# Kernel optimization log

Measured on AMD Instinct MI355X. Metric: run time of the kernel, lower is better.

The kernel has to match this reference:

```python
import jax, jax.numpy as jnp
import numpy as np

B, S, D, H = 2, 2048, 1024, 16
ND = D // H  # head dim = 64


def setup_inputs() -> dict:
    key = jax.random.key(0)
    ks = jax.random.split(key, 11)
    scale = 1.0 / np.sqrt(D)
    inp = {
        "q": jax.random.normal(ks[0], (B, S, D), dtype=jnp.float32),
        "k": jax.random.normal(ks[1], (B, S, D), dtype=jnp.float32),
        "v": jax.random.normal(ks[2], (B, S, D), dtype=jnp.float32),
        # causal mask, broadcast over batch and heads
        "mask": jnp.tril(jnp.ones((S, S), dtype=jnp.int32))[None, None, :, :],
        "Wq": jax.random.normal(ks[3], (D, D), dtype=jnp.float32) * scale,
        "bq": jnp.zeros((D,), dtype=jnp.float32),
        "Wk": jax.random.normal(ks[4], (D, D), dtype=jnp.float32) * scale,
        "bk": jnp.zeros((D,), dtype=jnp.float32),
        "Wv": jax.random.normal(ks[5], (D, D), dtype=jnp.float32) * scale,
        "bv": jnp.zeros((D,), dtype=jnp.float32),
        "Wo": jax.random.normal(ks[6], (D, D), dtype=jnp.float32) * scale,
        "bo": jnp.zeros((D,), dtype=jnp.float32),
    }
    return inp


def reference(q, k, v, mask, Wq, bq, Wk, bk, Wv, bv, Wo, bo):
    batch, seq_len, _ = q.shape
    # torch nn.Linear: x @ W.T + b
    qh = (q @ Wq.T + bq).reshape(batch, seq_len, H, ND).transpose(0, 2, 1, 3)
    kh = (k @ Wk.T + bk).reshape(batch, seq_len, H, ND).transpose(0, 2, 1, 3)
    vh = (v @ Wv.T + bv).reshape(batch, seq_len, H, ND).transpose(0, 2, 1, 3)
    # [B,H,S,S] scores
    score = jnp.einsum("bhqd,bhkd->bhqk", qh, kh) / jnp.sqrt(jnp.float32(ND))
    score = jnp.where(mask == 0, jnp.float32(-1e9), score)
    score = jax.nn.softmax(score, axis=-1)
    out = jnp.einsum("bhqk,bhkd->bhqd", score, vh)
    out = out.transpose(0, 2, 1, 3).reshape(batch, seq_len, D)
    return out @ Wo.T + bo
```

## Files before the change

kernel.cpp:

```cpp
#include <hip/hip_runtime.h>
#include <hip/hip_bf16.h>
#include <stdint.h>

#define S_LEN 2048
#define DMODEL 1024
#define NHEAD 16
#define HDIM 64
#define BATCH 2

typedef __bf16 bf16_t;
typedef __attribute__((ext_vector_type(8))) __bf16 bf16x8;
typedef __attribute__((ext_vector_type(4))) __bf16 bf16x4;
typedef __attribute__((ext_vector_type(4))) float f32x4;

#define LOG2E 1.44269504088896340736f

__device__ __forceinline__ void gload_lds16(const void* g, void* l) {
  __builtin_amdgcn_global_load_lds(
      (const __attribute__((address_space(1))) uint32_t*)g,
      (__attribute__((address_space(3))) uint32_t*)l, 16, 0, 0);
}

__global__ __launch_bounds__(256) void convert_all(
    const float* __restrict__ q, const float* __restrict__ k, const float* __restrict__ v,
    const float* __restrict__ wq, const float* __restrict__ wk, const float* __restrict__ wv,
    const float* __restrict__ wo,
    bf16_t* __restrict__ qb, bf16_t* __restrict__ kb, bf16_t* __restrict__ vb,
    bf16_t* __restrict__ wqb, bf16_t* __restrict__ wkb, bf16_t* __restrict__ wvb,
    bf16_t* __restrict__ wob)
{
  const size_t M1 = 1048576;
  size_t e = ((size_t)blockIdx.x * 256 + threadIdx.x) * 4;
  const float* src; bf16_t* dst; size_t off;
  if      (e <  4*M1) { src = q;  dst = qb;  off = e;         }
  else if (e <  8*M1) { src = k;  dst = kb;  off = e - 4*M1;  }
  else if (e < 12*M1) { src = v;  dst = vb;  off = e - 8*M1;  }
  else if (e < 13*M1) { src = wq; dst = wqb; off = e - 12*M1; }
  else if (e < 14*M1) { src = wk; dst = wkb; off = e - 13*M1; }
  else if (e < 15*M1) { src = wv; dst = wvb; off = e - 14*M1; }
  else                { src = wo; dst = wob; off = e - 15*M1; }
  float4 f = *reinterpret_cast<const float4*>(src + off);
  bf16x4 o;
  o[0] = (bf16_t)f.x; o[1] = (bf16_t)f.y; o[2] = (bf16_t)f.z; o[3] = (bf16_t)f.w;
  *reinterpret_cast<bf16x4*>(dst + off) = o;
}

__device__ __forceinline__ void gemm_body(
    const bf16_t* __restrict__ A, const bf16_t* __restrict__ W,
    const float* __restrict__ bias, bf16_t* __restrict__ outb,
    float* __restrict__ outf, int M, int N, int K, float scale, int packmode)
{
  __shared__ bf16_t As[128 * 32];
  __shared__ bf16_t Bs[128 * 32];
  int tid = threadIdx.x;
  int w = tid >> 6, lane = tid & 63;
  int lr = lane & 15, lg = lane >> 4;
  int wr = w >> 1, wc = w & 1;
  int m0 = blockIdx.x * 128, n0 = blockIdx.y * 128;

  f32x4 acc[4][4];
#pragma unroll
  for (int a = 0; a < 4; ++a)
#pragma unroll
    for (int bq = 0; bq < 4; ++bq) acc[a][bq] = (f32x4){0.f, 0.f, 0.f, 0.f};

  int col_st = (lane & 3) * 8;

  for (int kt = 0; kt < K; kt += 32) {
#pragma unroll
    for (int it = 0; it < 2; ++it) {
      int chunkbase = (w * 2 + it) * 512;
      int row = (w * 2 + it) * 16 + (lane >> 2);
      gload_lds16(A + (size_t)(m0 + row) * K + kt + col_st, &As[chunkbase]);
      gload_lds16(W + (size_t)(n0 + row) * K + kt + col_st, &Bs[chunkbase]);
    }
    __syncthreads();
    bf16x8 af[4], bfv[4];
#pragma unroll
    for (int mf = 0; mf < 4; ++mf)
      af[mf] = *reinterpret_cast<const bf16x8*>(&As[(wr * 64 + mf * 16 + lr) * 32 + lg * 8]);
#pragma unroll
    for (int nf = 0; nf < 4; ++nf)
      bfv[nf] = *reinterpret_cast<const bf16x8*>(&Bs[(wc * 64 + nf * 16 + lr) * 32 + lg * 8]);
#pragma unroll
    for (int mf = 0; mf < 4; ++mf)
#pragma unroll
      for (int nf = 0; nf < 4; ++nf)
        acc[mf][nf] = __builtin_amdgcn_mfma_f32_16x16x32_bf16(af[mf], bfv[nf], acc[mf][nf], 0, 0, 0);
    __syncthreads();
  }

#pragma unroll
  for (int mf = 0; mf < 4; ++mf) {
#pragma unroll
    for (int nf = 0; nf < 4; ++nf) {
      int col = n0 + wc * 64 + nf * 16 + lr;
      float bcol = bias[col];
#pragma unroll
      for (int i = 0; i < 4; ++i) {
        int row = m0 + wr * 64 + mf * 16 + lg * 4 + i;
        float vv = (acc[mf][nf][i] + bcol) * scale;
        if (outf) {
          outf[(size_t)row * N + col] = vv;
        } else if (packmode == 0) {
          outb[(size_t)row * N + col] = (bf16_t)vv;
        } else if (packmode == 1) {
          int hh = col >> 6, dh = col & 63;
          int half = dh >> 5, klg = (dh >> 3) & 3, j = dh & 7;
          int bb = row >> 11, s = row & 2047;
          size_t off = ((((size_t)(bb * 16 + hh) * 32 + (s >> 6)) * 4 + ((s >> 4) & 3)) * 2 + half) * 512
                     + (klg * 16 + (s & 15)) * 8 + j;
          outb[off] = (bf16_t)vv;
        } else {
          int hh = col >> 6, d = col & 63;
          int dfo = d >> 4, vlr = d & 15;
          int bb = row >> 11, s = row & 2047;
          int t64 = s >> 6, sin_ = s & 63;
          int half = sin_ >> 5, vlg = (sin_ >> 3) & 3, j = s & 7;
          size_t off = (((size_t)(bb * 16 + hh) * 32 + t64) * 8 + dfo * 2 + half) * 512
                     + (vlg * 16 + vlr) * 8 + j;
          outb[off] = (bf16_t)vv;
        }
      }
    }
  }
}

__global__ __launch_bounds__(256) void gemm_proj(
    const bf16_t* __restrict__ qb, const bf16_t* __restrict__ kb, const bf16_t* __restrict__ vb,
    const bf16_t* __restrict__ wqb, const bf16_t* __restrict__ wkb, const bf16_t* __restrict__ wvb,
    const float* __restrict__ bq, const float* __restrict__ bk, const float* __restrict__ bv,
    bf16_t* __restrict__ Qp, bf16_t* __restrict__ Kpk, bf16_t* __restrict__ Vpk)
{
  int z = blockIdx.z;
  const bf16_t* A = (z == 0) ? qb : (z == 1) ? kb : vb;
  const bf16_t* W = (z == 0) ? wqb : (z == 1) ? wkb : wvb;
  const float* bias = (z == 0) ? bq : (z == 1) ? bk : bv;
  bf16_t* o = (z == 0) ? Qp : (z == 1) ? Kpk : Vpk;
  float scale = (z == 0) ? 0.125f * LOG2E : 1.0f;
  gemm_body(A, W, bias, o, nullptr, BATCH * S_LEN, DMODEL, DMODEL, scale, z);
}

__global__ __launch_bounds__(256) void gemm_out(
    const bf16_t* __restrict__ O, const bf16_t* __restrict__ wob,
    const float* __restrict__ bo, float* __restrict__ out)
{
  gemm_body(O, wob, bo, nullptr, out, BATCH * S_LEN, DMODEL, DMODEL, 1.0f, 0);
}

#define PSTRIDE 66

__global__ __launch_bounds__(512, 2) void attn_fwd(
    const bf16_t* __restrict__ Qp, const bf16_t* __restrict__ Kpk,
    const bf16_t* __restrict__ Vpk, bf16_t* __restrict__ O)
{
  int flat = blockIdx.x;
  int bh = flat & 31, j = flat >> 5;
  int b = bh >> 4, h = bh & 15;
  int tid = threadIdx.x, wv = tid >> 6, lane = tid & 63;
  int lr = lane & 15, lg = lane >> 4;
  int grp = wv >> 2, wl = wv & 3;

  __shared__ bf16_t Ps[8][2][16 * PSTRIDE];

  int qtile = grp ? (15 - j) : j;
  int rbase = qtile * 128 + wl * 32;
  int t_end = (rbase + 31) >> 6;

  bf16x8 qf[2][2];
#pragma unroll
  for (int g = 0; g < 2; ++g) {
    const bf16_t* Qb = Qp + ((size_t)b * S_LEN + rbase + g * 16 + lr) * DMODEL + h * HDIM + lg * 8;
    qf[g][0] = *reinterpret_cast<const bf16x8*>(Qb);
    qf[g][1] = *reinterpret_cast<const bf16x8*>(Qb + 32);
  }

  f32x4 oacc0[4], oacc1[4];
#pragma unroll
  for (int df = 0; df < 4; ++df) {
    oacc0[df] = (f32x4){0.f, 0.f, 0.f, 0.f};
    oacc1[df] = (f32x4){0.f, 0.f, 0.f, 0.f};
  }
  float m0 = -1e30f, l0 = 0.f, m1 = -1e30f, l1 = 0.f;

  const bf16_t* Kb = Kpk + (size_t)bh * (32 * 4096) + lane * 8;
  const bf16_t* Vb = Vpk + (size_t)bh * (32 * 4096) + lane * 8;
  bf16_t* ps0 = &Ps[wv][0][lr * PSTRIDE];
  bf16_t* ps1 = &Ps[wv][1][lr * PSTRIDE];

  for (int t = 0; t <= t_end; ++t) {
    const bf16_t* Kt = Kb + t * 4096;
    const bf16_t* Vt_ = Vb + t * 4096;

    bf16x8 kf[8];
#pragma unroll
    for (int f = 0; f < 8; ++f)
      kf[f] = *reinterpret_cast<const bf16x8*>(Kt + f * 512);
    bf16x8 vf[8];
#pragma unroll
    for (int f = 0; f < 8; ++f)
      vf[f] = *reinterpret_cast<const bf16x8*>(Vt_ + f * 512);

    f32x4 sa0[4], sa1[4];
    __builtin_amdgcn_s_setprio(1);
#pragma unroll
    for (int kvf = 0; kvf < 4; ++kvf) {
      f32x4 s = (f32x4){0.f, 0.f, 0.f, 0.f};
      s = __builtin_amdgcn_mfma_f32_16x16x32_bf16(kf[kvf * 2 + 0], qf[0][0], s, 0, 0, 0);
      s = __builtin_amdgcn_mfma_f32_16x16x32_bf16(kf[kvf * 2 + 1], qf[0][1], s, 0, 0, 0);
      sa0[kvf] = s;
      f32x4 s2 = (f32x4){0.f, 0.f, 0.f, 0.f};
      s2 = __builtin_amdgcn_mfma_f32_16x16x32_bf16(kf[kvf * 2 + 0], qf[1][0], s2, 0, 0, 0);
      s2 = __builtin_amdgcn_mfma_f32_16x16x32_bf16(kf[kvf * 2 + 1], qf[1][1], s2, 0, 0, 0);
      sa1[kvf] = s2;
    }
    __builtin_amdgcn_s_setprio(0);

    if (t == t_end) {
      int kv0 = t * 64;
#pragma unroll
      for (int kvf = 0; kvf < 4; ++kvf) {
        int kv_g = kv0 + kvf * 16 + lg * 4;
#pragma unroll
        for (int i = 0; i < 4; ++i) {
          if (kv_g + i > rbase + lr)      sa0[kvf][i] = -1e30f;
          if (kv_g + i > rbase + 16 + lr) sa1[kvf][i] = -1e30f;
        }
      }
    }

    {
      float lmax = fmaxf(fmaxf(sa0[0][0], sa0[0][1]), fmaxf(sa0[0][2], sa0[0][3]));
#pragma unroll
      for (int kvf = 1; kvf < 4; ++kvf)
        lmax = fmaxf(lmax, fmaxf(fmaxf(sa0[kvf][0], sa0[kvf][1]),
                                 fmaxf(sa0[kvf][2], sa0[kvf][3])));
      if (__any(lmax > m0 + 8.f)) {
        float mx = lmax;
        mx = fmaxf(mx, __shfl_xor(mx, 16));
        mx = fmaxf(mx, __shfl_xor(mx, 32));
        float mn = fmaxf(m0, mx);
        float rsc = __builtin_amdgcn_exp2f(m0 - mn);
        m0 = mn; l0 *= rsc;
#pragma unroll
        for (int dfo = 0; dfo < 4; ++dfo) oacc0[dfo] *= rsc;
      }
      float psum = 0.f;
#pragma unroll
      for (int kvf = 0; kvf < 4; ++kvf) {
        bf16x4 pw;
#pragma unroll
        for (int i = 0; i < 4; ++i) {
          float p = __builtin_amdgcn_exp2f(sa0[kvf][i] - m0);
          psum += p;
          pw[i] = (bf16_t)p;
        }
        *reinterpret_cast<bf16x4*>(ps0 + kvf * 16 + lg * 4) = pw;
      }
      l0 += psum;
    }
    {
      float lmax = fmaxf(fmaxf(sa1[0][0], sa1[0][1]), fmaxf(sa1[0][2], sa1[0][3]));
#pragma unroll
      for (int kvf = 1; kvf < 4; ++kvf)
        lmax = fmaxf(lmax, fmaxf(fmaxf(sa1[kvf][0], sa1[kvf][1]),
                                 fmaxf(sa1[kvf][2], sa1[kvf][3])));
      if (__any(lmax > m1 + 8.f)) {
        float mx = lmax;
        mx = fmaxf(mx, __shfl_xor(mx, 16));
        mx = fmaxf(mx, __shfl_xor(mx, 32));
        float mn = fmaxf(m1, mx);
        float rsc = __builtin_amdgcn_exp2f(m1 - mn);
        m1 = mn; l1 *= rsc;
#pragma unroll
        for (int dfo = 0; dfo < 4; ++dfo) oacc1[dfo] *= rsc;
      }
      float psum = 0.f;
#pragma unroll
      for (int kvf = 0; kvf < 4; ++kvf) {
        bf16x4 pw;
#pragma unroll
        for (int i = 0; i < 4; ++i) {
          float p = __builtin_amdgcn_exp2f(sa1[kvf][i] - m1);
          psum += p;
          pw[i] = (bf16_t)p;
        }
        *reinterpret_cast<bf16x4*>(ps1 + kvf * 16 + lg * 4) = pw;
      }
      l1 += psum;
    }

    asm volatile("s_waitcnt lgkmcnt(0)" ::: "memory");
    __builtin_amdgcn_sched_barrier(0);

    bf16x8 pa00 = *reinterpret_cast<const bf16x8*>(ps0 + lg * 8);
    bf16x8 pa01 = *reinterpret_cast<const bf16x8*>(ps0 + 32 + lg * 8);
    bf16x8 pa10 = *reinterpret_cast<const bf16x8*>(ps1 + lg * 8);
    bf16x8 pa11 = *reinterpret_cast<const bf16x8*>(ps1 + 32 + lg * 8);
    __builtin_amdgcn_s_setprio(1);
#pragma unroll
    for (int dfo = 0; dfo < 4; ++dfo) {
      oacc0[dfo] = __builtin_amdgcn_mfma_f32_16x16x32_bf16(vf[dfo * 2 + 0], pa00, oacc0[dfo], 0, 0, 0);
      oacc0[dfo] = __builtin_amdgcn_mfma_f32_16x16x32_bf16(vf[dfo * 2 + 1], pa01, oacc0[dfo], 0, 0, 0);
      oacc1[dfo] = __builtin_amdgcn_mfma_f32_16x16x32_bf16(vf[dfo * 2 + 0], pa10, oacc1[dfo], 0, 0, 0);
      oacc1[dfo] = __builtin_amdgcn_mfma_f32_16x16x32_bf16(vf[dfo * 2 + 1], pa11, oacc1[dfo], 0, 0, 0);
    }
    __builtin_amdgcn_s_setprio(0);
  }

  l0 += __shfl_xor(l0, 16);
  l0 += __shfl_xor(l0, 32);
  l1 += __shfl_xor(l1, 16);
  l1 += __shfl_xor(l1, 32);
  float inv0 = 1.0f / l0, inv1 = 1.0f / l1;
  bf16_t* ob0 = O + ((size_t)b * S_LEN + rbase + lr) * DMODEL + h * HDIM + lg * 4;
  bf16_t* ob1 = O + ((size_t)b * S_LEN + rbase + 16 + lr) * DMODEL + h * HDIM + lg * 4;
#pragma unroll
  for (int dfo = 0; dfo < 4; ++dfo) {
    bf16x4 ov0, ov1;
#pragma unroll
    for (int i = 0; i < 4; ++i) {
      ov0[i] = (bf16_t)(oacc0[dfo][i] * inv0);
      ov1[i] = (bf16_t)(oacc1[dfo][i] * inv1);
    }
    *reinterpret_cast<bf16x4*>(ob0 + dfo * 16) = ov0;
    *reinterpret_cast<bf16x4*>(ob1 + dfo * 16) = ov1;
  }
}

extern "C" void kernel_launch(void* const* d_in, const int* in_sizes, int n_in,
                              void* d_out, int out_size, void* d_ws, size_t ws_size,
                              hipStream_t stream) {
  const float* q  = (const float*)d_in[0];
  const float* k  = (const float*)d_in[1];
  const float* v  = (const float*)d_in[2];
  const float* Wq = (const float*)d_in[4];
  const float* bq = (const float*)d_in[5];
  const float* Wk = (const float*)d_in[6];
  const float* bk = (const float*)d_in[7];
  const float* Wv = (const float*)d_in[8];
  const float* bv = (const float*)d_in[9];
  const float* Wo = (const float*)d_in[10];
  const float* bo = (const float*)d_in[11];
  float* out = (float*)d_out;

  const size_t MB = 1u << 20;
  char* base = (char*)d_ws;
  bf16_t* qb  = (bf16_t*)(base + 0 * MB);
  bf16_t* kb  = (bf16_t*)(base + 8 * MB);
  bf16_t* vb  = (bf16_t*)(base + 16 * MB);
  bf16_t* wqb = (bf16_t*)(base + 24 * MB);
  bf16_t* wkb = (bf16_t*)(base + 26 * MB);
  bf16_t* wvb = (bf16_t*)(base + 28 * MB);
  bf16_t* wob = (bf16_t*)(base + 30 * MB);
  bf16_t* Qp  = (bf16_t*)(base + 32 * MB);
  bf16_t* Kpk = (bf16_t*)(base + 40 * MB);
  bf16_t* Vpk = (bf16_t*)(base + 56 * MB);
  bf16_t* Ob  = (bf16_t*)(base + 64 * MB);

  convert_all<<<16384, 256, 0, stream>>>(q, k, v, Wq, Wk, Wv, Wo,
                                         qb, kb, vb, wqb, wkb, wvb, wob);
  gemm_proj<<<dim3(32, 8, 3), 256, 0, stream>>>(qb, kb, vb, wqb, wkb, wvb,
                                                bq, bk, bv, Qp, Kpk, Vpk);
  attn_fwd<<<256, 512, 0, stream>>>(Qp, Kpk, Vpk, Ob);
  gemm_out<<<dim3(32, 8), 256, 0, stream>>>(Ob, wob, bo, out);
}
```

Before: 134.0 us.

## Fuse fp32-to-bf16 conversion into GEMM tile loads and drop convert kernel

Removes the separate conversion kernel that turned q/k/v and all weight matrices into bf16 copies in workspace. The projection and output GEMMs now read fp32 inputs and weights directly, convert in registers, and store bf16 into LDS, replacing the direct global-to-LDS loads. The goal is to save a full read/write pass over about 64MB of inputs plus one kernel launch. In exchange, each GEMM tile reads twice as many bytes from global memory or L2 and routes loads through registers, which may expose more load latency.

```diff
diff --git a/kernel.cpp b/kernel.cpp
--- a/kernel.cpp
+++ b/kernel.cpp
@@ -15,38 +15,9 @@
 
 #define LOG2E 1.44269504088896340736f
 
-__device__ __forceinline__ void gload_lds16(const void* g, void* l) {
-  __builtin_amdgcn_global_load_lds(
-      (const __attribute__((address_space(1))) uint32_t*)g,
-      (__attribute__((address_space(3))) uint32_t*)l, 16, 0, 0);
-}
-
-__global__ __launch_bounds__(256) void convert_all(
-    const float* __restrict__ q, const float* __restrict__ k, const float* __restrict__ v,
-    const float* __restrict__ wq, const float* __restrict__ wk, const float* __restrict__ wv,
-    const float* __restrict__ wo,
-    bf16_t* __restrict__ qb, bf16_t* __restrict__ kb, bf16_t* __restrict__ vb,
-    bf16_t* __restrict__ wqb, bf16_t* __restrict__ wkb, bf16_t* __restrict__ wvb,
-    bf16_t* __restrict__ wob)
-{
-  const size_t M1 = 1048576;
-  size_t e = ((size_t)blockIdx.x * 256 + threadIdx.x) * 4;
-  const float* src; bf16_t* dst; size_t off;
-  if      (e <  4*M1) { src = q;  dst = qb;  off = e;         }
-  else if (e <  8*M1) { src = k;  dst = kb;  off = e - 4*M1;  }
-  else if (e < 12*M1) { src = v;  dst = vb;  off = e - 8*M1;  }
-  else if (e < 13*M1) { src = wq; dst = wqb; off = e - 12*M1; }
-  else if (e < 14*M1) { src = wk; dst = wkb; off = e - 13*M1; }
-  else if (e < 15*M1) { src = wv; dst = wvb; off = e - 14*M1; }
-  else                { src = wo; dst = wob; off = e - 15*M1; }
-  float4 f = *reinterpret_cast<const float4*>(src + off);
-  bf16x4 o;
-  o[0] = (bf16_t)f.x; o[1] = (bf16_t)f.y; o[2] = (bf16_t)f.z; o[3] = (bf16_t)f.w;
-  *reinterpret_cast<bf16x4*>(dst + off) = o;
-}
-
+template <bool A_F32>
 __device__ __forceinline__ void gemm_body(
-    const bf16_t* __restrict__ A, const bf16_t* __restrict__ W,
+    const void* __restrict__ Araw, const float* __restrict__ Wf,
     const float* __restrict__ bias, bf16_t* __restrict__ outb,
     float* __restrict__ outf, int M, int N, int K, float scale, int packmode)
 {
@@ -71,8 +42,29 @@
     for (int it = 0; it < 2; ++it) {
       int chunkbase = (w * 2 + it) * 512;
       int row = (w * 2 + it) * 16 + (lane >> 2);
-      gload_lds16(A + (size_t)(m0 + row) * K + kt + col_st, &As[chunkbase]);
-      gload_lds16(W + (size_t)(n0 + row) * K + kt + col_st, &Bs[chunkbase]);
+      {
+        bf16x8 o;
+        if constexpr (A_F32) {
+          const float* ap = (const float*)Araw + (size_t)(m0 + row) * K + kt + col_st;
+          float4 a0 = *reinterpret_cast<const float4*>(ap);
+          float4 a1 = *reinterpret_cast<const float4*>(ap + 4);
+          o[0] = (bf16_t)a0.x; o[1] = (bf16_t)a0.y; o[2] = (bf16_t)a0.z; o[3] = (bf16_t)a0.w;
+          o[4] = (bf16_t)a1.x; o[5] = (bf16_t)a1.y; o[6] = (bf16_t)a1.z; o[7] = (bf16_t)a1.w;
+        } else {
+          o = *reinterpret_cast<const bf16x8*>(
+              (const bf16_t*)Araw + (size_t)(m0 + row) * K + kt + col_st);
+        }
+        *reinterpret_cast<bf16x8*>(&As[chunkbase + lane * 8]) = o;
+      }
+      {
+        const float* wp = Wf + (size_t)(n0 + row) * K + kt + col_st;
+        float4 w0 = *reinterpret_cast<const float4*>(wp);
+        float4 w1 = *reinterpret_cast<const float4*>(wp + 4);
+        bf16x8 o;
+        o[0] = (bf16_t)w0.x; o[1] = (bf16_t)w0.y; o[2] = (bf16_t)w0.z; o[3] = (bf16_t)w0.w;
+        o[4] = (bf16_t)w1.x; o[5] = (bf16_t)w1.y; o[6] = (bf16_t)w1.z; o[7] = (bf16_t)w1.w;
+        *reinterpret_cast<bf16x8*>(&Bs[chunkbase + lane * 8]) = o;
+      }
     }
     __syncthreads();
     bf16x8 af[4], bfv[4];
@@ -127,25 +119,25 @@
 }
 
 __global__ __launch_bounds__(256) void gemm_proj(
-    const bf16_t* __restrict__ qb, const bf16_t* __restrict__ kb, const bf16_t* __restrict__ vb,
-    const bf16_t* __restrict__ wqb, const bf16_t* __restrict__ wkb, const bf16_t* __restrict__ wvb,
+    const float* __restrict__ q, const float* __restrict__ k, const float* __restrict__ v,
+    const float* __restrict__ wq, const float* __restrict__ wk, const float* __restrict__ wv,
     const float* __restrict__ bq, const float* __restrict__ bk, const float* __restrict__ bv,
     bf16_t* __restrict__ Qp, bf16_t* __restrict__ Kpk, bf16_t* __restrict__ Vpk)
 {
   int z = blockIdx.z;
-  const bf16_t* A = (z == 0) ? qb : (z == 1) ? kb : vb;
-  const bf16_t* W = (z == 0) ? wqb : (z == 1) ? wkb : wvb;
+  const float* A = (z == 0) ? q : (z == 1) ? k : v;
+  const float* W = (z == 0) ? wq : (z == 1) ? wk : wv;
   const float* bias = (z == 0) ? bq : (z == 1) ? bk : bv;
   bf16_t* o = (z == 0) ? Qp : (z == 1) ? Kpk : Vpk;
   float scale = (z == 0) ? 0.125f * LOG2E : 1.0f;
-  gemm_body(A, W, bias, o, nullptr, BATCH * S_LEN, DMODEL, DMODEL, scale, z);
+  gemm_body<true>(A, W, bias, o, nullptr, BATCH * S_LEN, DMODEL, DMODEL, scale, z);
 }
 
 __global__ __launch_bounds__(256) void gemm_out(
-    const bf16_t* __restrict__ O, const bf16_t* __restrict__ wob,
+    const bf16_t* __restrict__ O, const float* __restrict__ wo,
     const float* __restrict__ bo, float* __restrict__ out)
 {
-  gemm_body(O, wob, bo, nullptr, out, BATCH * S_LEN, DMODEL, DMODEL, 1.0f, 0);
+  gemm_body<false>(O, wo, bo, nullptr, out, BATCH * S_LEN, DMODEL, DMODEL, 1.0f, 0);
 }
 
 #define PSTRIDE 66
@@ -346,22 +338,13 @@
 
   const size_t MB = 1u << 20;
   char* base = (char*)d_ws;
-  bf16_t* qb  = (bf16_t*)(base + 0 * MB);
-  bf16_t* kb  = (bf16_t*)(base + 8 * MB);
-  bf16_t* vb  = (bf16_t*)(base + 16 * MB);
-  bf16_t* wqb = (bf16_t*)(base + 24 * MB);
-  bf16_t* wkb = (bf16_t*)(base + 26 * MB);
-  bf16_t* wvb = (bf16_t*)(base + 28 * MB);
-  bf16_t* wob = (bf16_t*)(base + 30 * MB);
-  bf16_t* Qp  = (bf16_t*)(base + 32 * MB);
-  bf16_t* Kpk = (bf16_t*)(base + 40 * MB);
-  bf16_t* Vpk = (bf16_t*)(base + 56 * MB);
-  bf16_t* Ob  = (bf16_t*)(base + 64 * MB);
-
-  convert_all<<<16384, 256, 0, stream>>>(q, k, v, Wq, Wk, Wv, Wo,
-                                         qb, kb, vb, wqb, wkb, wvb, wob);
-  gemm_proj<<<dim3(32, 8, 3), 256, 0, stream>>>(qb, kb, vb, wqb, wkb, wvb,
+  bf16_t* Qp  = (bf16_t*)(base + 0 * MB);
+  bf16_t* Kpk = (bf16_t*)(base + 8 * MB);
+  bf16_t* Vpk = (bf16_t*)(base + 16 * MB);
+  bf16_t* Ob  = (bf16_t*)(base + 24 * MB);
+
+  gemm_proj<<<dim3(32, 8, 3), 256, 0, stream>>>(q, k, v, Wq, Wk, Wv,
                                                 bq, bk, bv, Qp, Kpk, Vpk);
   attn_fwd<<<256, 512, 0, stream>>>(Qp, Kpk, Vpk, Ob);
-  gemm_out<<<dim3(32, 8), 256, 0, stream>>>(Ob, wob, bo, out);
-}
+  gemm_out<<<dim3(32, 8), 256, 0, stream>>>(Ob, Wo, bo, out);
+}
```

After: 140.4 us. 4.8% more time.

## Split attention KV range across wave pairs with LDS merge of partial softmax

Applied to the files above, without the earlier changes.

Attention now launches 512 blocks of 256 threads. Each block handles two 64-row query tiles in turn, pairing tile qp with 31-qp to balance the causal work. Within a tile, two waves split the KV loop in half, and their partial max, sum and output are merged through shared memory in a flash-decoding-style combine. This shortens the serial KV chain per wave and raises parallelism, at the cost of extra LDS traffic, two syncthreads per tile, and redundant Q loads. Workspace offsets for Vpk and Ob are also compacted.

```diff
diff --git a/kernel.cpp b/kernel.cpp
--- a/kernel.cpp
+++ b/kernel.cpp
@@ -150,181 +150,229 @@
 
 #define PSTRIDE 66
 
-__global__ __launch_bounds__(512, 2) void attn_fwd(
+__global__ __launch_bounds__(256, 2) void attn_fwd(
     const bf16_t* __restrict__ Qp, const bf16_t* __restrict__ Kpk,
     const bf16_t* __restrict__ Vpk, bf16_t* __restrict__ O)
 {
   int flat = blockIdx.x;
-  int bh = flat & 31, j = flat >> 5;
+  int bh = flat & 31, qp = flat >> 5;
   int b = bh >> 4, h = bh & 15;
   int tid = threadIdx.x, wv = tid >> 6, lane = tid & 63;
   int lr = lane & 15, lg = lane >> 4;
-  int grp = wv >> 2, wl = wv & 3;
-
-  __shared__ bf16_t Ps[8][2][16 * PSTRIDE];
-
-  int qtile = grp ? (15 - j) : j;
-  int rbase = qtile * 128 + wl * 32;
-  int t_end = (rbase + 31) >> 6;
-
-  bf16x8 qf[2][2];
-#pragma unroll
-  for (int g = 0; g < 2; ++g) {
-    const bf16_t* Qb = Qp + ((size_t)b * S_LEN + rbase + g * 16 + lr) * DMODEL + h * HDIM + lg * 8;
-    qf[g][0] = *reinterpret_cast<const bf16x8*>(Qb);
-    qf[g][1] = *reinterpret_cast<const bf16x8*>(Qb + 32);
-  }
-
-  f32x4 oacc0[4], oacc1[4];
-#pragma unroll
-  for (int df = 0; df < 4; ++df) {
-    oacc0[df] = (f32x4){0.f, 0.f, 0.f, 0.f};
-    oacc1[df] = (f32x4){0.f, 0.f, 0.f, 0.f};
-  }
-  float m0 = -1e30f, l0 = 0.f, m1 = -1e30f, l1 = 0.f;
+  int s = wv >> 1, hf = wv & 1;
+
+  __shared__ bf16_t Ps[4][2][16 * PSTRIDE];
+  __shared__ float Mm[2][2][64];
+  __shared__ float Lm[2][2][64];
+  __shared__ float Om[2][2][64][17];
 
   const bf16_t* Kb = Kpk + (size_t)bh * (32 * 4096) + lane * 8;
   const bf16_t* Vb = Vpk + (size_t)bh * (32 * 4096) + lane * 8;
   bf16_t* ps0 = &Ps[wv][0][lr * PSTRIDE];
   bf16_t* ps1 = &Ps[wv][1][lr * PSTRIDE];
 
-  for (int t = 0; t <= t_end; ++t) {
-    const bf16_t* Kt = Kb + t * 4096;
-    const bf16_t* Vt_ = Vb + t * 4096;
-
-    bf16x8 kf[8];
-#pragma unroll
-    for (int f = 0; f < 8; ++f)
-      kf[f] = *reinterpret_cast<const bf16x8*>(Kt + f * 512);
-    bf16x8 vf[8];
-#pragma unroll
-    for (int f = 0; f < 8; ++f)
-      vf[f] = *reinterpret_cast<const bf16x8*>(Vt_ + f * 512);
-
-    f32x4 sa0[4], sa1[4];
-    __builtin_amdgcn_s_setprio(1);
-#pragma unroll
-    for (int kvf = 0; kvf < 4; ++kvf) {
-      f32x4 s = (f32x4){0.f, 0.f, 0.f, 0.f};
-      s = __builtin_amdgcn_mfma_f32_16x16x32_bf16(kf[kvf * 2 + 0], qf[0][0], s, 0, 0, 0);
-      s = __builtin_amdgcn_mfma_f32_16x16x32_bf16(kf[kvf * 2 + 1], qf[0][1], s, 0, 0, 0);
-      sa0[kvf] = s;
-      f32x4 s2 = (f32x4){0.f, 0.f, 0.f, 0.f};
-      s2 = __builtin_amdgcn_mfma_f32_16x16x32_bf16(kf[kvf * 2 + 0], qf[1][0], s2, 0, 0, 0);
-      s2 = __builtin_amdgcn_mfma_f32_16x16x32_bf16(kf[kvf * 2 + 1], qf[1][1], s2, 0, 0, 0);
-      sa1[kvf] = s2;
-    }
-    __builtin_amdgcn_s_setprio(0);
-
-    if (t == t_end) {
-      int kv0 = t * 64;
+  for (int p = 0; p < 2; ++p) {
+    int qt = p ? (31 - qp) : qp;
+    int rbase = qt * 64 + s * 32;
+    int nt = qt + 1;
+    int hsp = (nt + 1) >> 1;
+    int t0 = hf ? hsp : 0;
+    int t1 = hf ? nt : hsp;
+
+    bf16x8 qf[2][2];
+#pragma unroll
+    for (int g = 0; g < 2; ++g) {
+      const bf16_t* Qb = Qp + ((size_t)b * S_LEN + rbase + g * 16 + lr) * DMODEL + h * HDIM + lg * 8;
+      qf[g][0] = *reinterpret_cast<const bf16x8*>(Qb);
+      qf[g][1] = *reinterpret_cast<const bf16x8*>(Qb + 32);
+    }
+
+    f32x4 oacc0[4], oacc1[4];
+#pragma unroll
+    for (int df = 0; df < 4; ++df) {
+      oacc0[df] = (f32x4){0.f, 0.f, 0.f, 0.f};
+      oacc1[df] = (f32x4){0.f, 0.f, 0.f, 0.f};
+    }
+    float m0 = -1e30f, l0 = 0.f, m1 = -1e30f, l1 = 0.f;
+
+    for (int t = t0; t < t1; ++t) {
+      const bf16_t* Kt = Kb + t * 4096;
+      const bf16_t* Vt_ = Vb + t * 4096;
+
+      bf16x8 kf[8];
+#pragma unroll
+      for (int f = 0; f < 8; ++f)
+        kf[f] = *reinterpret_cast<const bf16x8*>(Kt + f * 512);
+      bf16x8 vf[8];
+#pragma unroll
+      for (int f = 0; f < 8; ++f)
+        vf[f] = *reinterpret_cast<const bf16x8*>(Vt_ + f * 512);
+
+      f32x4 sa0[4], sa1[4];
+      __builtin_amdgcn_s_setprio(1);
 #pragma unroll
       for (int kvf = 0; kvf < 4; ++kvf) {
-        int kv_g = kv0 + kvf * 16 + lg * 4;
+        f32x4 sv = (f32x4){0.f, 0.f, 0.f, 0.f};
+        sv = __builtin_amdgcn_mfma_f32_16x16x32_bf16(kf[kvf * 2 + 0], qf[0][0], sv, 0, 0, 0);
+        sv = __builtin_amdgcn_mfma_f32_16x16x32_bf16(kf[kvf * 2 + 1], qf[0][1], sv, 0, 0, 0);
+        sa0[kvf] = sv;
+        f32x4 sv2 = (f32x4){0.f, 0.f, 0.f, 0.f};
+        sv2 = __builtin_amdgcn_mfma_f32_16x16x32_bf16(kf[kvf * 2 + 0], qf[1][0], sv2, 0, 0, 0);
+        sv2 = __builtin_amdgcn_mfma_f32_16x16x32_bf16(kf[kvf * 2 + 1], qf[1][1], sv2, 0, 0, 0);
+        sa1[kvf] = sv2;
+      }
+      __builtin_amdgcn_s_setprio(0);
+
+      if (t == qt) {
+        int kv0 = t * 64;
+#pragma unroll
+        for (int kvf = 0; kvf < 4; ++kvf) {
+          int kv_g = kv0 + kvf * 16 + lg * 4;
+#pragma unroll
+          for (int i = 0; i < 4; ++i) {
+            if (kv_g + i > rbase + lr)      sa0[kvf][i] = -1e30f;
+            if (kv_g + i > rbase + 16 + lr) sa1[kvf][i] = -1e30f;
+          }
+        }
+      }
+
+      {
+        float lmax = fmaxf(fmaxf(sa0[0][0], sa0[0][1]), fmaxf(sa0[0][2], sa0[0][3]));
+#pragma unroll
+        for (int kvf = 1; kvf < 4; ++kvf)
+          lmax = fmaxf(lmax, fmaxf(fmaxf(sa0[kvf][0], sa0[kvf][1]),
+                                   fmaxf(sa0[kvf][2], sa0[kvf][3])));
+        if (__any(lmax > m0 + 8.f)) {
+          float mx = lmax;
+          mx = fmaxf(mx, __shfl_xor(mx, 16));
+          mx = fmaxf(mx, __shfl_xor(mx, 32));
+          float mn = fmaxf(m0, mx);
+          float rsc = __builtin_amdgcn_exp2f(m0 - mn);
+          m0 = mn; l0 *= rsc;
+#pragma unroll
+          for (int dfo = 0; dfo < 4; ++dfo) oacc0[dfo] *= rsc;
+        }
+        float psum = 0.f;
+#pragma unroll
+        for (int kvf = 0; kvf < 4; ++kvf) {
+          bf16x4 pw;
+#pragma unroll
+          for (int i = 0; i < 4; ++i) {
+            float pe = __builtin_amdgcn_exp2f(sa0[kvf][i] - m0);
+            psum += pe;
+            pw[i] = (bf16_t)pe;
+          }
+          *reinterpret_cast<bf16x4*>(ps0 + kvf * 16 + lg * 4) = pw;
+        }
+        l0 += psum;
+      }
+      {
+        float lmax = fmaxf(fmaxf(sa1[0][0], sa1[0][1]), fmaxf(sa1[0][2], sa1[0][3]));
+#pragma unroll
+        for (int kvf = 1; kvf < 4; ++kvf)
+          lmax = fmaxf(lmax, fmaxf(fmaxf(sa1[kvf][0], sa1[kvf][1]),
+                                   fmaxf(sa1[kvf][2], sa1[kvf][3])));
+        if (__any(lmax > m1 + 8.f)) {
+          float mx = lmax;
+          mx = fmaxf(mx, __shfl_xor(mx, 16));
+          mx = fmaxf(mx, __shfl_xor(mx, 32));
+          float mn = fmaxf(m1, mx);
+          float rsc = __builtin_amdgcn_exp2f(m1 - mn);
+          m1 = mn; l1 *= rsc;
+#pragma unroll
+          for (int dfo = 0; dfo < 4; ++dfo) oacc1[dfo] *= rsc;
+        }
+        float psum = 0.f;
+#pragma unroll
+        for (int kvf = 0; kvf < 4; ++kvf) {
+          bf16x4 pw;
+#pragma unroll
+          for (int i = 0; i < 4; ++i) {
+            float pe = __builtin_amdgcn_exp2f(sa1[kvf][i] - m1);
+            psum += pe;
+            pw[i] = (bf16_t)pe;
+          }
+          *reinterpret_cast<bf16x4*>(ps1 + kvf * 16 + lg * 4) = pw;
+        }
+        l1 += psum;
+      }
+
+      asm volatile("s_waitcnt lgkmcnt(0)" ::: "memory");
+      __builtin_amdgcn_sched_barrier(0);
+
+      bf16x8 pa00 = *reinterpret_cast<const bf16x8*>(ps0 + lg * 8);
+      bf16x8 pa01 = *reinterpret_cast<const bf16x8*>(ps0 + 32 + lg * 8);
+      bf16x8 pa10 = *reinterpret_cast<const bf16x8*>(ps1 + lg * 8);
+      bf16x8 pa11 = *reinterpret_cast<const bf16x8*>(ps1 + 32 + lg * 8);
+      __builtin_amdgcn_s_setprio(1);
+#pragma unroll
+      for (int dfo = 0; dfo < 4; ++dfo) {
+        oacc0[dfo] = __builtin_amdgcn_mfma_f32_16x16x32_bf16(vf[dfo * 2 + 0], pa00, oacc0[dfo], 0, 0, 0);
+        oacc0[dfo] = __builtin_amdgcn_mfma_f32_16x16x32_bf16(vf[dfo * 2 + 1], pa01, oacc0[dfo], 0, 0, 0);
+        oacc1[dfo] = __builtin_amdgcn_mfma_f32_16x16x32_bf16(vf[dfo * 2 + 0], pa10, oacc1[dfo], 0, 0, 0);
+        oacc1[dfo] = __builtin_amdgcn_mfma_f32_16x16x32_bf16(vf[dfo * 2 + 1], pa11, oacc1[dfo], 0, 0, 0);
+      }
+      __builtin_amdgcn_s_setprio(0);
+    }
+
+    if (hf) {
+      Mm[s][0][lane] = m0; Lm[s][0][lane] = l0;
+      Mm[s][1][lane] = m1; Lm[s][1][lane] = l1;
+#pragma unroll
+      for (int dfo = 0; dfo < 4; ++dfo)
 #pragma unroll
         for (int i = 0; i < 4; ++i) {
-          if (kv_g + i > rbase + lr)      sa0[kvf][i] = -1e30f;
-          if (kv_g + i > rbase + 16 + lr) sa1[kvf][i] = -1e30f;
-        }
-      }
-    }
-
-    {
-      float lmax = fmaxf(fmaxf(sa0[0][0], sa0[0][1]), fmaxf(sa0[0][2], sa0[0][3]));
-#pragma unroll
-      for (int kvf = 1; kvf < 4; ++kvf)
-        lmax = fmaxf(lmax, fmaxf(fmaxf(sa0[kvf][0], sa0[kvf][1]),
-                                 fmaxf(sa0[kvf][2], sa0[kvf][3])));
-      if (__any(lmax > m0 + 8.f)) {
-        float mx = lmax;
-        mx = fmaxf(mx, __shfl_xor(mx, 16));
-        mx = fmaxf(mx, __shfl_xor(mx, 32));
-        float mn = fmaxf(m0, mx);
-        float rsc = __builtin_amdgcn_exp2f(m0 - mn);
-        m0 = mn; l0 *= rsc;
-#pragma unroll
-        for (int dfo = 0; dfo < 4; ++dfo) oacc0[dfo] *= rsc;
-      }
-      float psum = 0.f;
-#pragma unroll
-      for (int kvf = 0; kvf < 4; ++kvf) {
-        bf16x4 pw;
+          Om[s][0][lane][dfo * 4 + i] = oacc0[dfo][i];
+          Om[s][1][lane][dfo * 4 + i] = oacc1[dfo][i];
+        }
+    }
+    __syncthreads();
+    if (!hf) {
+      {
+        float mB = Mm[s][0][lane], lB = Lm[s][0][lane];
+        float mAB = fmaxf(m0, mB);
+        float fA = __builtin_amdgcn_exp2f(m0 - mAB);
+        float fB = __builtin_amdgcn_exp2f(mB - mAB);
+        l0 = l0 * fA + lB * fB;
+#pragma unroll
+        for (int dfo = 0; dfo < 4; ++dfo)
+#pragma unroll
+          for (int i = 0; i < 4; ++i)
+            oacc0[dfo][i] = oacc0[dfo][i] * fA + Om[s][0][lane][dfo * 4 + i] * fB;
+      }
+      {
+        float mB = Mm[s][1][lane], lB = Lm[s][1][lane];
+        float mAB = fmaxf(m1, mB);
+        float fA = __builtin_amdgcn_exp2f(m1 - mAB);
+        float fB = __builtin_amdgcn_exp2f(mB - mAB);
+        l1 = l1 * fA + lB * fB;
+#pragma unroll
+        for (int dfo = 0; dfo < 4; ++dfo)
+#pragma unroll
+          for (int i = 0; i < 4; ++i)
+            oacc1[dfo][i] = oacc1[dfo][i] * fA + Om[s][1][lane][dfo * 4 + i] * fB;
+      }
+
+      l0 += __shfl_xor(l0, 16);
+      l0 += __shfl_xor(l0, 32);
+      l1 += __shfl_xor(l1, 16);
+      l1 += __shfl_xor(l1, 32);
+      float inv0 = 1.0f / l0, inv1 = 1.0f / l1;
+      bf16_t* ob0 = O + ((size_t)b * S_LEN + rbase + lr) * DMODEL + h * HDIM + lg * 4;
+      bf16_t* ob1 = O + ((size_t)b * S_LEN + rbase + 16 + lr) * DMODEL + h * HDIM + lg * 4;
+#pragma unroll
+      for (int dfo = 0; dfo < 4; ++dfo) {
+        bf16x4 ov0, ov1;
 #pragma unroll
         for (int i = 0; i < 4; ++i) {
-          float p = __builtin_amdgcn_exp2f(sa0[kvf][i] - m0);
-          psum += p;
-          pw[i] = (bf16_t)p;
-        }
-        *reinterpret_cast<bf16x4*>(ps0 + kvf * 16 + lg * 4) = pw;
-      }
-      l0 += psum;
-    }
-    {
-      float lmax = fmaxf(fmaxf(sa1[0][0], sa1[0][1]), fmaxf(sa1[0][2], sa1[0][3]));
-#pragma unroll
-      for (int kvf = 1; kvf < 4; ++kvf)
-        lmax = fmaxf(lmax, fmaxf(fmaxf(sa1[kvf][0], sa1[kvf][1]),
-                                 fmaxf(sa1[kvf][2], sa1[kvf][3])));
-      if (__any(lmax > m1 + 8.f)) {
-        float mx = lmax;
-        mx = fmaxf(mx, __shfl_xor(mx, 16));
-        mx = fmaxf(mx, __shfl_xor(mx, 32));
-        float mn = fmaxf(m1, mx);
-        float rsc = __builtin_amdgcn_exp2f(m1 - mn);
-        m1 = mn; l1 *= rsc;
-#pragma unroll
-        for (int dfo = 0; dfo < 4; ++dfo) oacc1[dfo] *= rsc;
-      }
-      float psum = 0.f;
-#pragma unroll
-      for (int kvf = 0; kvf < 4; ++kvf) {
-        bf16x4 pw;
-#pragma unroll
-        for (int i = 0; i < 4; ++i) {
-          float p = __builtin_amdgcn_exp2f(sa1[kvf][i] - m1);
-          psum += p;
-          pw[i] = (bf16_t)p;
-        }
-        *reinterpret_cast<bf16x4*>(ps1 + kvf * 16 + lg * 4) = pw;
-      }
-      l1 += psum;
-    }
-
-    asm volatile("s_waitcnt lgkmcnt(0)" ::: "memory");
-    __builtin_amdgcn_sched_barrier(0);
-
-    bf16x8 pa00 = *reinterpret_cast<const bf16x8*>(ps0 + lg * 8);
-    bf16x8 pa01 = *reinterpret_cast<const bf16x8*>(ps0 + 32 + lg * 8);
-    bf16x8 pa10 = *reinterpret_cast<const bf16x8*>(ps1 + lg * 8);
-    bf16x8 pa11 = *reinterpret_cast<const bf16x8*>(ps1 + 32 + lg * 8);
-    __builtin_amdgcn_s_setprio(1);
-#pragma unroll
-    for (int dfo = 0; dfo < 4; ++dfo) {
-      oacc0[dfo] = __builtin_amdgcn_mfma_f32_16x16x32_bf16(vf[dfo * 2 + 0], pa00, oacc0[dfo], 0, 0, 0);
-      oacc0[dfo] = __builtin_amdgcn_mfma_f32_16x16x32_bf16(vf[dfo * 2 + 1], pa01, oacc0[dfo], 0, 0, 0);
-      oacc1[dfo] = __builtin_amdgcn_mfma_f32_16x16x32_bf16(vf[dfo * 2 + 0], pa10, oacc1[dfo], 0, 0, 0);
-      oacc1[dfo] = __builtin_amdgcn_mfma_f32_16x16x32_bf16(vf[dfo * 2 + 1], pa11, oacc1[dfo], 0, 0, 0);
-    }
-    __builtin_amdgcn_s_setprio(0);
-  }
-
-  l0 += __shfl_xor(l0, 16);
-  l0 += __shfl_xor(l0, 32);
-  l1 += __shfl_xor(l1, 16);
-  l1 += __shfl_xor(l1, 32);
-  float inv0 = 1.0f / l0, inv1 = 1.0f / l1;
-  bf16_t* ob0 = O + ((size_t)b * S_LEN + rbase + lr) * DMODEL + h * HDIM + lg * 4;
-  bf16_t* ob1 = O + ((size_t)b * S_LEN + rbase + 16 + lr) * DMODEL + h * HDIM + lg * 4;
-#pragma unroll
-  for (int dfo = 0; dfo < 4; ++dfo) {
-    bf16x4 ov0, ov1;
-#pragma unroll
-    for (int i = 0; i < 4; ++i) {
-      ov0[i] = (bf16_t)(oacc0[dfo][i] * inv0);
-      ov1[i] = (bf16_t)(oacc1[dfo][i] * inv1);
-    }
-    *reinterpret_cast<bf16x4*>(ob0 + dfo * 16) = ov0;
-    *reinterpret_cast<bf16x4*>(ob1 + dfo * 16) = ov1;
+          ov0[i] = (bf16_t)(oacc0[dfo][i] * inv0);
+          ov1[i] = (bf16_t)(oacc1[dfo][i] * inv1);
+        }
+        *reinterpret_cast<bf16x4*>(ob0 + dfo * 16) = ov0;
+        *reinterpret_cast<bf16x4*>(ob1 + dfo * 16) = ov1;
+      }
+    }
+    __syncthreads();
   }
 }
 
@@ -355,13 +403,13 @@
   bf16_t* wob = (bf16_t*)(base + 30 * MB);
   bf16_t* Qp  = (bf16_t*)(base + 32 * MB);
   bf16_t* Kpk = (bf16_t*)(base + 40 * MB);
-  bf16_t* Vpk = (bf16_t*)(base + 56 * MB);
-  bf16_t* Ob  = (bf16_t*)(base + 64 * MB);
+  bf16_t* Vpk = (bf16_t*)(base + 48 * MB);
+  bf16_t* Ob  = (bf16_t*)(base + 56 * MB);
 
   convert_all<<<16384, 256, 0, stream>>>(q, k, v, Wq, Wk, Wv, Wo,
                                          qb, kb, vb, wqb, wkb, wvb, wob);
   gemm_proj<<<dim3(32, 8, 3), 256, 0, stream>>>(qb, kb, vb, wqb, wkb, wvb,
                                                 bq, bk, bv, Qp, Kpk, Vpk);
-  attn_fwd<<<256, 512, 0, stream>>>(Qp, Kpk, Vpk, Ob);
+  attn_fwd<<<512, 256, 0, stream>>>(Qp, Kpk, Vpk, Ob);
   gemm_out<<<dim3(32, 8), 256, 0, stream>>>(Ob, wob, bo, out);
 }
```

New measurement: 132.0 us. No clear change (-1.5%).
